# Performance work log

Hardware: AMD Instinct MI355X
Metric: run time of the kernel (lower is better)

The kernel has to match this reference:

```python
import jax, jax.numpy as jnp
import numpy as np

WS = 7       # window size
SHIFT = 3    # shift size
NH = 6       # num heads

def layernorm(x, w, b, eps=1e-5):
    mu = jnp.mean(x, axis=-1, keepdims=True)
    var = jnp.var(x, axis=-1, keepdims=True)
    return (x - mu) * jax.lax.rsqrt(var + eps) * w + b

def setup_inputs() -> dict:
    key = jax.random.key(0)
    ks = jax.random.split(key, 8)
    B, H, W, C = 16, 56, 56, 192
    hid = 4 * C
    s = lambda k, shape, fan: jax.random.normal(k, shape, jnp.float32) * (fan ** -0.5)
    return {
        "x": jax.random.normal(ks[0], (B, H, W, C), jnp.float32),
        "ln1_w": jnp.ones((C,), jnp.float32), "ln1_b": jnp.zeros((C,), jnp.float32),
        "qkv_w": s(ks[1], (C, 3 * C), C), "qkv_b": jnp.zeros((3 * C,), jnp.float32),
        "proj_w": s(ks[2], (C, C), C), "proj_b": jnp.zeros((C,), jnp.float32),
        "ln2_w": jnp.ones((C,), jnp.float32), "ln2_b": jnp.zeros((C,), jnp.float32),
        "mlp_w1": s(ks[3], (C, hid), C), "mlp_b1": jnp.zeros((hid,), jnp.float32),
        "mlp_w2": s(ks[4], (hid, C), hid), "mlp_b2": jnp.zeros((C,), jnp.float32),
    }

def reference(x, ln1_w, ln1_b, qkv_w, qkv_b, proj_w, proj_b, ln2_w, ln2_b, mlp_w1, mlp_b1, mlp_w2, mlp_b2):
    B, H, W, C = x.shape
    hd = C // NH
    scale = hd ** -0.5
    N = WS * WS

    shortcut = x
    xn = layernorm(x, ln1_w, ln1_b)
    # cyclic shift
    xs = jnp.roll(xn, shift=(-SHIFT, -SHIFT), axis=(1, 2))
    # window partition: [B*nW, N, C]
    xw = xs.reshape(B, H // WS, WS, W // WS, WS, C)
    xw = xw.transpose(0, 1, 3, 2, 4, 5).reshape(-1, N, C)

    # window attention
    qkv = xw @ qkv_w + qkv_b                       # [Bn, N, 3C]
    qkv = qkv.reshape(-1, N, 3, NH, hd).transpose(2, 0, 3, 1, 4)  # [3, Bn, NH, N, hd]
    q, k, v = qkv[0], qkv[1], qkv[2]
    attn = jnp.einsum('bhqd,bhkd->bhqk', q, k) * scale
    attn = jax.nn.softmax(attn, axis=-1)
    o = jnp.einsum('bhqk,bhkd->bhqd', attn, v)     # [Bn, NH, N, hd]
    o = o.transpose(0, 2, 1, 3).reshape(-1, N, C)
    o = o @ proj_w + proj_b

    # window reverse
    o = o.reshape(B, H // WS, W // WS, WS, WS, C)
    o = o.transpose(0, 1, 3, 2, 4, 5).reshape(B, H, W, C)
    # reverse shift
    o = jnp.roll(o, shift=(SHIFT, SHIFT), axis=(1, 2))

    x = shortcut + o
    # MLP (exact GELU, matching torch nn.GELU default)
    h = layernorm(x, ln2_w, ln2_b)
    h = jax.nn.gelu(h @ mlp_w1 + mlp_b1, approximate=False)
    x = x + (h @ mlp_w2 + mlp_b2)
    return x
```

## Files before the change

kernel.cpp:

```cpp
#include <hip/hip_runtime.h>
#include <hip/hip_bf16.h>
#include <math.h>

typedef __attribute__((ext_vector_type(8))) short short8;
typedef __attribute__((ext_vector_type(4))) float float4v;
typedef __attribute__((ext_vector_type(2))) unsigned int uint2v;

#define C_DIM 192
#define NHEADS 6
#define NTOK 50176

__device__ __forceinline__ float bf2f(unsigned short u){
  union { unsigned int i; float f; } x; x.i = ((unsigned int)u) << 16; return x.f;
}
__device__ __forceinline__ unsigned short f2bf(float f){
  union { float f; unsigned int i; } x; x.f = f;
  unsigned int r = x.i + 0x7fff + ((x.i >> 16) & 1);
  return (unsigned short)(r >> 16);
}
__device__ __forceinline__ unsigned int rbf(float f){
  union { float f; unsigned int i; } x; x.f = f;
  return x.i + 0x7fff + ((x.i >> 16) & 1);
}
__device__ __forceinline__ unsigned int pack_bf2(float lo, float hi){
  return __builtin_amdgcn_perm(rbf(hi), rbf(lo), 0x07060302);
}

__device__ __forceinline__ void gload_lds16(const unsigned short* g, unsigned short* l){
  __builtin_amdgcn_global_load_lds((const __attribute__((address_space(1))) void*)g,
                                   (__attribute__((address_space(3))) void*)l, 16, 0, 0);
}

__device__ __forceinline__ int nat_token(int r){
  int win = r / 49, n = r - win * 49;
  int b = win >> 6, rem = win & 63;
  int hs = (rem >> 3) * 7 + n / 7;
  int ws = (rem & 7) * 7 + n % 7;
  int h = hs + 3; if (h >= 56) h -= 56;
  int w = ws + 3; if (w >= 56) w -= 56;
  return (b * 56 + h) * 56 + w;
}

__device__ __forceinline__ float gelu_f(float v){
  float t = v * v;
  float u = fmaf(0.1029436f, t, 2.302208f);
  float e = __builtin_amdgcn_exp2f(-v * u);
  return v * __builtin_amdgcn_rcpf(1.f + e);
}

__global__ void transpose_kernel(const float* __restrict__ in,
                                 unsigned short* __restrict__ out, int R, int Cc){
  int idx = blockIdx.x * 256 + threadIdx.x;
  if (idx < R * Cc){ int r = idx / Cc, c = idx - r * Cc; out[(long)c * R + r] = f2bf(in[idx]); }
}

__global__ __launch_bounds__(256) void ln1_kernel(const float* __restrict__ x,
                                                  const float* __restrict__ w,
                                                  const float* __restrict__ b,
                                                  unsigned short* __restrict__ out){
  int wave = threadIdx.x >> 6, lane = threadIdx.x & 63;
  int r = blockIdx.x * 4 + wave;
  int src = nat_token(r);
  const float* xp = x + (long)src * C_DIM;
  float v0 = xp[lane], v1 = xp[lane + 64], v2 = xp[lane + 128];
  float s = v0 + v1 + v2, s2 = v0*v0 + v1*v1 + v2*v2;
  for (int m = 32; m >= 1; m >>= 1){ s += __shfl_xor(s, m, 64); s2 += __shfl_xor(s2, m, 64); }
  float mean = s * (1.f/192.f);
  float var  = s2 * (1.f/192.f) - mean*mean;
  float rs = rsqrtf(var + 1e-5f);
  unsigned short* op = out + (long)r * C_DIM;
  op[lane]       = f2bf((v0-mean)*rs*w[lane]       + b[lane]);
  op[lane + 64]  = f2bf((v1-mean)*rs*w[lane + 64]  + b[lane + 64]);
  op[lane + 128] = f2bf((v2-mean)*rs*w[lane + 128] + b[lane + 128]);
}

__global__ __launch_bounds__(256) void attn_kernel(const unsigned short* __restrict__ qkv,
                                                   unsigned short* __restrict__ o){
  __shared__ unsigned short pbuf[4][64][72];
  int wave = threadIdx.x >> 6, lane = threadIdx.x & 63;
  int quad = lane >> 4, l16 = lane & 15;
  int wid = blockIdx.x * 4 + wave;
  int win = wid / NHEADS, head = wid - win * NHEADS;
  const unsigned short* qp = qkv + (long)win * 49 * 576 + head * 32;
  const unsigned short* kp = qp + 192;
  const unsigned short* vp = qp + 384;

  short8 qa[4], kb[4];
  #pragma unroll
  for (int mi = 0; mi < 4; mi++){
    int m = mi * 16 + l16; if (m > 48) m = 48;
    qa[mi] = *(const short8*)&qp[(long)m * 576 + quad * 8];
  }
  #pragma unroll
  for (int ni = 0; ni < 4; ni++){
    int n = ni * 16 + l16; if (n > 48) n = 48;
    kb[ni] = *(const short8*)&kp[(long)n * 576 + quad * 8];
  }
  float4v S[4][4];
  #pragma unroll
  for (int mi = 0; mi < 4; mi++)
    #pragma unroll
    for (int ni = 0; ni < 4; ni++) S[mi][ni] = (float4v)0.f;
  #pragma unroll
  for (int mi = 0; mi < 4; mi++)
    #pragma unroll
    for (int ni = 0; ni < 4; ni++)
      S[mi][ni] = __builtin_amdgcn_mfma_f32_16x16x32_bf16(qa[mi], kb[ni], S[mi][ni], 0, 0, 0);

  #pragma unroll
  for (int mi = 0; mi < 4; mi++){
    #pragma unroll
    for (int r = 0; r < 4; r++){
      float e[4];
      float sum = 0.f;
      #pragma unroll
      for (int ni = 0; ni < 4; ni++){
        int n = ni * 16 + l16;
        float s = S[mi][ni][r] * 0.17677669529663687f;
        s = fminf(s, 80.f);
        float ev = (n <= 48) ? __expf(s) : 0.f;
        e[ni] = ev; sum += ev;
      }
      sum += __shfl_xor(sum, 1, 64);
      sum += __shfl_xor(sum, 2, 64);
      sum += __shfl_xor(sum, 4, 64);
      sum += __shfl_xor(sum, 8, 64);
      float inv = 1.f / sum;
      int m = mi * 16 + quad * 4 + r;
      #pragma unroll
      for (int ni = 0; ni < 4; ni++)
        pbuf[wave][m][ni * 16 + l16] = f2bf(e[ni] * inv);
    }
  }
  __syncthreads();

  short8 vb[2][2];
  #pragma unroll
  for (int kk2 = 0; kk2 < 2; kk2++){
    #pragma unroll
    for (int ni = 0; ni < 2; ni++){
      union { unsigned short us[8]; short8 v8; } u;
      #pragma unroll
      for (int j = 0; j < 8; j++){
        int k = kk2 * 32 + quad * 8 + j; if (k > 48) k = 48;
        u.us[j] = vp[(long)k * 576 + ni * 16 + l16];
      }
      vb[kk2][ni] = u.v8;
    }
  }

  float4v O[4][2];
  #pragma unroll
  for (int mi = 0; mi < 4; mi++)
    #pragma unroll
    for (int ni = 0; ni < 2; ni++) O[mi][ni] = (float4v)0.f;
  #pragma unroll
  for (int kk2 = 0; kk2 < 2; kk2++){
    short8 pa[4];
    #pragma unroll
    for (int mi = 0; mi < 4; mi++)
      pa[mi] = *(const short8*)&pbuf[wave][mi * 16 + l16][kk2 * 32 + quad * 8];
    #pragma unroll
    for (int mi = 0; mi < 4; mi++)
      #pragma unroll
      for (int ni = 0; ni < 2; ni++)
        O[mi][ni] = __builtin_amdgcn_mfma_f32_16x16x32_bf16(pa[mi], vb[kk2][ni], O[mi][ni], 0, 0, 0);
  }

  #pragma unroll
  for (int mi = 0; mi < 4; mi++){
    int m0 = mi * 16 + quad * 4;
    #pragma unroll
    for (int r = 0; r < 4; r++){
      if (m0 + r <= 48){
        #pragma unroll
        for (int ni = 0; ni < 2; ni++)
          o[((long)win * 49 + m0 + r) * C_DIM + head * 32 + ni * 16 + l16] = f2bf(O[mi][ni][r]);
      }
    }
  }
}

template<int EPI>
__global__ __launch_bounds__(256) void gemm_kernel(const unsigned short* __restrict__ A,
                                                   const unsigned short* __restrict__ Bt,
                                                   const float* __restrict__ bias,
                                                   unsigned short* __restrict__ Cout,
                                                   float* __restrict__ Fout,
                                                   const float* __restrict__ Xres,
                                                   int N, int K){
  __shared__ unsigned short As[128 * 64];
  __shared__ unsigned short Bs[64 * 64];
  int tid = threadIdx.x;
  int wave = tid >> 6, lane = tid & 63, quad = lane >> 4, l16 = lane & 15;
  int wm = (wave >> 1) * 64, wn = (wave & 1) * 32;
  int lrow = lane >> 3, lg = lane & 7;
  int gcol = (lg ^ lrow) * 8;
  float4v acc[4][2];
  #pragma unroll
  for (int i = 0; i < 4; i++)
    #pragma unroll
    for (int jj = 0; jj < 2; jj++) acc[i][jj] = (float4v)0.f;

  long arow0 = (long)blockIdx.x * 128;
  long brow0 = (long)blockIdx.y * 64;
  int sw = (l16 & 7);

  for (int k0 = 0; k0 < K; k0 += 64){
    #pragma unroll
    for (int t = 0; t < 4; t++){
      int ci = wave + 4 * t;
      gload_lds16(&A[(arow0 + ci * 8 + lrow) * (long)K + k0 + gcol], &As[ci * 512]);
    }
    #pragma unroll
    for (int t = 0; t < 2; t++){
      int ci = wave + 4 * t;
      gload_lds16(&Bt[(brow0 + ci * 8 + lrow) * (long)K + k0 + gcol], &Bs[ci * 512]);
    }
    __syncthreads();
    #pragma unroll
    for (int kk8 = 0; kk8 < 8; kk8 += 4){
      short8 a[4], b[2];
      #pragma unroll
      for (int mi = 0; mi < 4; mi++)
        a[mi] = *(const short8*)&As[(wm + mi*16 + l16) * 64 + ((quad + kk8) ^ sw) * 8];
      #pragma unroll
      for (int ni = 0; ni < 2; ni++)
        b[ni] = *(const short8*)&Bs[(wn + ni*16 + l16) * 64 + ((quad + kk8) ^ sw) * 8];
      #pragma unroll
      for (int mi = 0; mi < 4; mi++)
        #pragma unroll
        for (int ni = 0; ni < 2; ni++)
          acc[mi][ni] = __builtin_amdgcn_mfma_f32_16x16x32_bf16(b[ni], a[mi], acc[mi][ni], 0, 0, 0);
    }
    __syncthreads();
  }

  float4v bias4[2];
  #pragma unroll
  for (int ni = 0; ni < 2; ni++)
    bias4[ni] = *(const float4v*)&bias[brow0 + wn + ni*16 + quad*4];

  #pragma unroll
  for (int mi = 0; mi < 4; mi++){
    long r = arow0 + wm + mi*16 + l16;
    long tr = (EPI == 1) ? (long)nat_token((int)r) : r;
    #pragma unroll
    for (int ni = 0; ni < 2; ni++){
      long c0 = brow0 + wn + ni*16 + quad*4;
      float4v v = acc[mi][ni] + bias4[ni];
      if (EPI == 0){
        uint2v pp;
        pp[0] = pack_bf2(v[0], v[1]);
        pp[1] = pack_bf2(v[2], v[3]);
        *(uint2v*)&Cout[r * N + c0] = pp;
      } else {
        long idx = tr * C_DIM + c0;
        float4v xr = *(const float4v*)&Xres[idx];
        *(float4v*)&Fout[idx] = xr + v;
      }
    }
  }
}

__global__ __launch_bounds__(256, 4) void gemm128_kernel(const unsigned short* __restrict__ A,
                                                         const unsigned short* __restrict__ Bt,
                                                         const float* __restrict__ bias,
                                                         unsigned short* __restrict__ Cout,
                                                         int N, int K){
  __shared__ unsigned short As[128 * 64];
  __shared__ unsigned short Bs[128 * 64];
  int tid = threadIdx.x;
  int wave = tid >> 6, lane = tid & 63, quad = lane >> 4, l16 = lane & 15;
  int wm = (wave >> 1) * 64, wn = (wave & 1) * 64;
  int lrow = lane >> 3, lg = lane & 7;
  int gcol = (lg ^ lrow) * 8;
  int sw = (l16 & 7);
  float4v acc[4][4];
  #pragma unroll
  for (int i = 0; i < 4; i++)
    #pragma unroll
    for (int jj = 0; jj < 4; jj++) acc[i][jj] = (float4v)0.f;

  long arow0 = (long)blockIdx.x * 128;
  long brow0 = (long)blockIdx.y * 128;

  for (int k0 = 0; k0 < K; k0 += 64){
    #pragma unroll
    for (int t = 0; t < 4; t++){
      int ci = wave + 4 * t;
      gload_lds16(&A[(arow0 + ci * 8 + lrow) * (long)K + k0 + gcol], &As[ci * 512]);
    }
    #pragma unroll
    for (int t = 0; t < 4; t++){
      int ci = wave + 4 * t;
      gload_lds16(&Bt[(brow0 + ci * 8 + lrow) * (long)K + k0 + gcol], &Bs[ci * 512]);
    }
    __syncthreads();
    #pragma unroll
    for (int kk8 = 0; kk8 < 8; kk8 += 4){
      short8 a[4], b[4];
      #pragma unroll
      for (int mi = 0; mi < 4; mi++)
        a[mi] = *(const short8*)&As[(wm + mi*16 + l16) * 64 + ((quad + kk8) ^ sw) * 8];
      #pragma unroll
      for (int ni = 0; ni < 4; ni++)
        b[ni] = *(const short8*)&Bs[(wn + ni*16 + l16) * 64 + ((quad + kk8) ^ sw) * 8];
      #pragma unroll
      for (int mi = 0; mi < 4; mi++)
        #pragma unroll
        for (int ni = 0; ni < 4; ni++)
          acc[mi][ni] = __builtin_amdgcn_mfma_f32_16x16x32_bf16(b[ni], a[mi], acc[mi][ni], 0, 0, 0);
    }
    __syncthreads();
  }

  float4v bias4[4];
  #pragma unroll
  for (int ni = 0; ni < 4; ni++)
    bias4[ni] = *(const float4v*)&bias[brow0 + wn + ni*16 + quad*4];

  #pragma unroll
  for (int mi = 0; mi < 4; mi++){
    long r = arow0 + wm + mi*16 + l16;
    #pragma unroll
    for (int ni = 0; ni < 4; ni++){
      long c0 = brow0 + wn + ni*16 + quad*4;
      float4v v = acc[mi][ni] + bias4[ni];
      #pragma unroll
      for (int e = 0; e < 4; e++) v[e] = gelu_f(v[e]);
      uint2v pp;
      pp[0] = pack_bf2(v[0], v[1]);
      pp[1] = pack_bf2(v[2], v[3]);
      *(uint2v*)&Cout[r * N + c0] = pp;
    }
  }
}

__global__ __launch_bounds__(512, 4) void proj_ln2_kernel(const unsigned short* __restrict__ A,
                                                          const unsigned short* __restrict__ Bt,
                                                          const float* __restrict__ bias,
                                                          const float* __restrict__ x,
                                                          float* __restrict__ y,
                                                          const float* __restrict__ lnw,
                                                          const float* __restrict__ lnb,
                                                          unsigned short* __restrict__ hn){
  __shared__ unsigned short As[64 * 64];
  __shared__ unsigned short Bs[192 * 64];
  __shared__ float lnred[2][2][16][4][2];
  int tid = threadIdx.x;
  int wave = tid >> 6, lane = tid & 63, quad = lane >> 4, l16 = lane & 15;
  int wr = wave >> 2, wc = wave & 3;
  int lrow = lane >> 3, lg = lane & 7;
  int gcol = (lg ^ lrow) * 8;
  int sw = (l16 & 7);
  long arow0 = (long)blockIdx.x * 64;

  float4v acc[2][3];
  #pragma unroll
  for (int i = 0; i < 2; i++)
    #pragma unroll
    for (int j = 0; j < 3; j++) acc[i][j] = (float4v)0.f;

  for (int k0 = 0; k0 < 192; k0 += 64){
    #pragma unroll
    for (int t = 0; t < 4; t++){
      int i = wave + 8 * t;
      if (i < 8){
        gload_lds16(&A[(arow0 + i * 8 + lrow) * 192 + k0 + gcol], &As[i * 512]);
      } else {
        int ci = i - 8;
        gload_lds16(&Bt[(ci * 8 + lrow) * 192 + k0 + gcol], &Bs[ci * 512]);
      }
    }
    __syncthreads();
    #pragma unroll
    for (int kk8 = 0; kk8 < 8; kk8 += 4){
      short8 a[2], b[3];
      #pragma unroll
      for (int mi = 0; mi < 2; mi++)
        a[mi] = *(const short8*)&As[(wr*32 + mi*16 + l16) * 64 + ((quad + kk8) ^ sw) * 8];
      #pragma unroll
      for (int ni = 0; ni < 3; ni++)
        b[ni] = *(const short8*)&Bs[(wc*48 + ni*16 + l16) * 64 + ((quad + kk8) ^ sw) * 8];
      #pragma unroll
      for (int mi = 0; mi < 2; mi++)
        #pragma unroll
        for (int ni = 0; ni < 3; ni++)
          acc[mi][ni] = __builtin_amdgcn_mfma_f32_16x16x32_bf16(b[ni], a[mi], acc[mi][ni], 0, 0, 0);
    }
    if (k0 < 128) __syncthreads();
  }

  float4v bias4[3];
  #pragma unroll
  for (int ni = 0; ni < 3; ni++)
    bias4[ni] = *(const float4v*)&bias[wc*48 + ni*16 + quad*4];

  #pragma unroll
  for (int mi = 0; mi < 2; mi++){
    long rwin = arow0 + wr*32 + mi*16 + l16;
    long t = nat_token((int)rwin);
    float s = 0.f, s2 = 0.f;
    #pragma unroll
    for (int ni = 0; ni < 3; ni++){
      long idx = t * C_DIM + wc*48 + ni*16 + quad*4;
      float4v xr = *(const float4v*)&x[idx];
      float4v v = acc[mi][ni] + bias4[ni] + xr;
      *(float4v*)&y[idx] = v;
      acc[mi][ni] = v;
      #pragma unroll
      for (int e = 0; e < 4; e++){ s += v[e]; s2 += v[e]*v[e]; }
    }
    s  += __shfl_xor(s, 16, 64);  s  += __shfl_xor(s, 32, 64);
    s2 += __shfl_xor(s2, 16, 64); s2 += __shfl_xor(s2, 32, 64);
    if (quad == 0){ lnred[wr][mi][l16][wc][0] = s; lnred[wr][mi][l16][wc][1] = s2; }
  }
  __syncthreads();

  #pragma unroll
  for (int mi = 0; mi < 2; mi++){
    long rwin = arow0 + wr*32 + mi*16 + l16;
    float S = 0.f, S2 = 0.f;
    #pragma unroll
    for (int w = 0; w < 4; w++){ S += lnred[wr][mi][l16][w][0]; S2 += lnred[wr][mi][l16][w][1]; }
    float mean = S * (1.f/192.f);
    float var  = S2 * (1.f/192.f) - mean*mean;
    float rs = rsqrtf(var + 1e-5f);
    #pragma unroll
    for (int ni = 0; ni < 3; ni++){
      int c0 = wc*48 + ni*16 + quad*4;
      float4v w4 = *(const float4v*)&lnw[c0];
      float4v b4 = *(const float4v*)&lnb[c0];
      float4v v = acc[mi][ni];
      float g0 = (v[0]-mean)*rs*w4[0] + b4[0];
      float g1 = (v[1]-mean)*rs*w4[1] + b4[1];
      float g2 = (v[2]-mean)*rs*w4[2] + b4[2];
      float g3 = (v[3]-mean)*rs*w4[3] + b4[3];
      uint2v pp;
      pp[0] = pack_bf2(g0, g1);
      pp[1] = pack_bf2(g2, g3);
      *(uint2v*)&hn[rwin * C_DIM + c0] = pp;
    }
  }
}

extern "C" void kernel_launch(void* const* d_in, const int* in_sizes, int n_in,
                              void* d_out, int out_size, void* d_ws, size_t ws_size,
                              hipStream_t stream){
  const float* x      = (const float*)d_in[0];
  const float* ln1_w  = (const float*)d_in[1];
  const float* ln1_b  = (const float*)d_in[2];
  const float* qkv_w  = (const float*)d_in[3];
  const float* qkv_b  = (const float*)d_in[4];
  const float* proj_w = (const float*)d_in[5];
  const float* proj_b = (const float*)d_in[6];
  const float* ln2_w  = (const float*)d_in[7];
  const float* ln2_b  = (const float*)d_in[8];
  const float* mlp_w1 = (const float*)d_in[9];
  const float* mlp_b1 = (const float*)d_in[10];
  const float* mlp_w2 = (const float*)d_in[11];
  const float* mlp_b2 = (const float*)d_in[12];
  float* out = (float*)d_out;

  char* ws = (char*)d_ws;
  unsigned short* qkv_wt = (unsigned short*)(ws);
  unsigned short* proj_wt= (unsigned short*)(ws + 221184);
  unsigned short* w1t    = (unsigned short*)(ws + 294912);
  unsigned short* w2t    = (unsigned short*)(ws + 589824);
  unsigned short* R1     = (unsigned short*)(ws + 884736);
  unsigned short* R0     = (unsigned short*)(ws + 20152320);

  unsigned short* xw   = R1;
  unsigned short* obuf = R1;
  unsigned short* hn   = R1;
  unsigned short* qkv  = R0;
  unsigned short* hbuf = R0;

  transpose_kernel<<<(110592 + 255) / 256, 256, 0, stream>>>(qkv_w, qkv_wt, 192, 576);
  transpose_kernel<<<(36864  + 255) / 256, 256, 0, stream>>>(proj_w, proj_wt, 192, 192);
  transpose_kernel<<<(147456 + 255) / 256, 256, 0, stream>>>(mlp_w1, w1t, 192, 768);
  transpose_kernel<<<(147456 + 255) / 256, 256, 0, stream>>>(mlp_w2, w2t, 768, 192);

  ln1_kernel<<<NTOK / 4, 256, 0, stream>>>(x, ln1_w, ln1_b, xw);
  gemm_kernel<0><<<dim3(392, 9), 256, 0, stream>>>(xw, qkv_wt, qkv_b, qkv, nullptr, nullptr, 576, 192);
  attn_kernel<<<(NTOK / 49) * NHEADS / 4, 256, 0, stream>>>(qkv, obuf);
  proj_ln2_kernel<<<NTOK / 64, 512, 0, stream>>>(obuf, proj_wt, proj_b, x, out, ln2_w, ln2_b, hn);
  gemm128_kernel<<<dim3(392, 6), 256, 0, stream>>>(hn, w1t, mlp_b1, hbuf, 768, 192);
  gemm_kernel<1><<<dim3(392, 3), 256, 0, stream>>>(hbuf, w2t, mlp_b2, nullptr, out, out, 192, 768);
}
```

Baseline: 279.2 us.

## Fuse MLP fc1+GELU and fc2 into one kernel keeping hidden tile in LDS

```diff
diff --git a/kernel.cpp b/kernel.cpp
--- a/kernel.cpp
+++ b/kernel.cpp
@@ -181,13 +181,10 @@
   }
 }
 
-template<int EPI>
 __global__ __launch_bounds__(256) void gemm_kernel(const unsigned short* __restrict__ A,
                                                    const unsigned short* __restrict__ Bt,
                                                    const float* __restrict__ bias,
                                                    unsigned short* __restrict__ Cout,
-                                                   float* __restrict__ Fout,
-                                                   const float* __restrict__ Xres,
                                                    int N, int K){
   __shared__ unsigned short As[128 * 64];
   __shared__ unsigned short Bs[64 * 64];
@@ -244,91 +241,10 @@
   #pragma unroll
   for (int mi = 0; mi < 4; mi++){
     long r = arow0 + wm + mi*16 + l16;
-    long tr = (EPI == 1) ? (long)nat_token((int)r) : r;
     #pragma unroll
     for (int ni = 0; ni < 2; ni++){
       long c0 = brow0 + wn + ni*16 + quad*4;
       float4v v = acc[mi][ni] + bias4[ni];
-      if (EPI == 0){
-        uint2v pp;
-        pp[0] = pack_bf2(v[0], v[1]);
-        pp[1] = pack_bf2(v[2], v[3]);
-        *(uint2v*)&Cout[r * N + c0] = pp;
-      } else {
-        long idx = tr * C_DIM + c0;
-        float4v xr = *(const float4v*)&Xres[idx];
-        *(float4v*)&Fout[idx] = xr + v;
-      }
-    }
-  }
-}
-
-__global__ __launch_bounds__(256, 4) void gemm128_kernel(const unsigned short* __restrict__ A,
-                                                         const unsigned short* __restrict__ Bt,
-                                                         const float* __restrict__ bias,
-                                                         unsigned short* __restrict__ Cout,
-                                                         int N, int K){
-  __shared__ unsigned short As[128 * 64];
-  __shared__ unsigned short Bs[128 * 64];
-  int tid = threadIdx.x;
-  int wave = tid >> 6, lane = tid & 63, quad = lane >> 4, l16 = lane & 15;
-  int wm = (wave >> 1) * 64, wn = (wave & 1) * 64;
-  int lrow = lane >> 3, lg = lane & 7;
-  int gcol = (lg ^ lrow) * 8;
-  int sw = (l16 & 7);
-  float4v acc[4][4];
-  #pragma unroll
-  for (int i = 0; i < 4; i++)
-    #pragma unroll
-    for (int jj = 0; jj < 4; jj++) acc[i][jj] = (float4v)0.f;
-
-  long arow0 = (long)blockIdx.x * 128;
-  long brow0 = (long)blockIdx.y * 128;
-
-  for (int k0 = 0; k0 < K; k0 += 64){
-    #pragma unroll
-    for (int t = 0; t < 4; t++){
-      int ci = wave + 4 * t;
-      gload_lds16(&A[(arow0 + ci * 8 + lrow) * (long)K + k0 + gcol], &As[ci * 512]);
-    }
-    #pragma unroll
-    for (int t = 0; t < 4; t++){
-      int ci = wave + 4 * t;
-      gload_lds16(&Bt[(brow0 + ci * 8 + lrow) * (long)K + k0 + gcol], &Bs[ci * 512]);
-    }
-    __syncthreads();
-    #pragma unroll
-    for (int kk8 = 0; kk8 < 8; kk8 += 4){
-      short8 a[4], b[4];
-      #pragma unroll
-      for (int mi = 0; mi < 4; mi++)
-        a[mi] = *(const short8*)&As[(wm + mi*16 + l16) * 64 + ((quad + kk8) ^ sw) * 8];
-      #pragma unroll
-      for (int ni = 0; ni < 4; ni++)
-        b[ni] = *(const short8*)&Bs[(wn + ni*16 + l16) * 64 + ((quad + kk8) ^ sw) * 8];
-      #pragma unroll
-      for (int mi = 0; mi < 4; mi++)
-        #pragma unroll
-        for (int ni = 0; ni < 4; ni++)
-          acc[mi][ni] = __builtin_amdgcn_mfma_f32_16x16x32_bf16(b[ni], a[mi], acc[mi][ni], 0, 0, 0);
-    }
-    __syncthreads();
-  }
-
-  float4v bias4[4];
-  #pragma unroll
-  for (int ni = 0; ni < 4; ni++)
-    bias4[ni] = *(const float4v*)&bias[brow0 + wn + ni*16 + quad*4];
-
-  #pragma unroll
-  for (int mi = 0; mi < 4; mi++){
-    long r = arow0 + wm + mi*16 + l16;
-    #pragma unroll
-    for (int ni = 0; ni < 4; ni++){
-      long c0 = brow0 + wn + ni*16 + quad*4;
-      float4v v = acc[mi][ni] + bias4[ni];
-      #pragma unroll
-      for (int e = 0; e < 4; e++) v[e] = gelu_f(v[e]);
       uint2v pp;
       pp[0] = pack_bf2(v[0], v[1]);
       pp[1] = pack_bf2(v[2], v[3]);
@@ -445,6 +361,111 @@
   }
 }
 
+__global__ __launch_bounds__(256, 4) void fused_mlp_kernel(const unsigned short* __restrict__ hn,
+                                                           const unsigned short* __restrict__ w1t,
+                                                           const float* __restrict__ b1,
+                                                           const unsigned short* __restrict__ w2t,
+                                                           const float* __restrict__ b2,
+                                                           float* __restrict__ y){
+  __shared__ __attribute__((aligned(16))) unsigned short As[3 * 64 * 64];
+  __shared__ __attribute__((aligned(16))) unsigned short Hs[64 * 72];
+  int tid = threadIdx.x;
+  int wave = tid >> 6, lane = tid & 63, quad = lane >> 4, l16 = lane & 15;
+  int wm = (wave >> 1) * 32;
+  int wn1 = (wave & 1) * 32;
+  int wn2 = (wave & 1) * 96;
+  int lrow = lane >> 3, lg = lane & 7;
+  int gcol = (lg ^ lrow) * 8;
+  int sw = l16 & 7;
+  long arow0 = (long)blockIdx.x * 64;
+
+  float4v acc2[2][6];
+  #pragma unroll
+  for (int i = 0; i < 2; i++)
+    #pragma unroll
+    for (int j = 0; j < 6; j++) acc2[i][j] = (float4v)0.f;
+
+  #pragma unroll
+  for (int t = 0; t < 6; t++){
+    int i = wave + 4 * t; int gg = i >> 3, br8 = (i & 7) << 3;
+    gload_lds16(&hn[(arow0 + br8 + lrow) * C_DIM + gg * 64 + gcol], &As[gg * 4096 + br8 * 64]);
+  }
+  __syncthreads();
+
+  #pragma unroll 1
+  for (int j = 0; j < 12; j++){
+    int c0 = j * 64;
+    float4v acc1[2][2];
+    #pragma unroll
+    for (int mi = 0; mi < 2; mi++)
+      #pragma unroll
+      for (int ni = 0; ni < 2; ni++) acc1[mi][ni] = (float4v)0.f;
+    #pragma unroll
+    for (int kk = 0; kk < 6; kk++){
+      int gg = kk >> 1, xb = (kk & 1) * 4;
+      short8 a[2];
+      #pragma unroll
+      for (int mi = 0; mi < 2; mi++)
+        a[mi] = *(const short8*)&As[gg * 4096 + (wm + mi*16 + l16) * 64 + ((xb + quad) ^ sw) * 8];
+      #pragma unroll
+      for (int ni = 0; ni < 2; ni++){
+        short8 b = *(const short8*)&w1t[(long)(c0 + wn1 + ni*16 + l16) * 192 + kk*32 + quad*8];
+        #pragma unroll
+        for (int mi = 0; mi < 2; mi++)
+          acc1[mi][ni] = __builtin_amdgcn_mfma_f32_16x16x32_bf16(b, a[mi], acc1[mi][ni], 0, 0, 0);
+      }
+    }
+    #pragma unroll
+    for (int ni = 0; ni < 2; ni++){
+      float4v b14 = *(const float4v*)&b1[c0 + wn1 + ni*16 + quad*4];
+      #pragma unroll
+      for (int mi = 0; mi < 2; mi++){
+        float4v v = acc1[mi][ni] + b14;
+        #pragma unroll
+        for (int e = 0; e < 4; e++) v[e] = gelu_f(v[e]);
+        uint2v pp;
+        pp[0] = pack_bf2(v[0], v[1]);
+        pp[1] = pack_bf2(v[2], v[3]);
+        *(uint2v*)&Hs[(wm + mi*16 + l16) * 72 + wn1 + ni*16 + quad*4] = pp;
+      }
+    }
+    __syncthreads();
+
+    #pragma unroll
+    for (int kk2 = 0; kk2 < 2; kk2++){
+      short8 pa[2];
+      #pragma unroll
+      for (int mi = 0; mi < 2; mi++)
+        pa[mi] = *(const short8*)&Hs[(wm + mi*16 + l16) * 72 + kk2*32 + quad*8];
+      #pragma unroll
+      for (int ni = 0; ni < 6; ni++){
+        short8 b = *(const short8*)&w2t[(long)(wn2 + ni*16 + l16) * 768 + c0 + kk2*32 + quad*8];
+        #pragma unroll
+        for (int mi = 0; mi < 2; mi++)
+          acc2[mi][ni] = __builtin_amdgcn_mfma_f32_16x16x32_bf16(b, pa[mi], acc2[mi][ni], 0, 0, 0);
+      }
+    }
+    __syncthreads();
+  }
+
+  float4v b24[6];
+  #pragma unroll
+  for (int ni = 0; ni < 6; ni++)
+    b24[ni] = *(const float4v*)&b2[wn2 + ni*16 + quad*4];
+
+  #pragma unroll
+  for (int mi = 0; mi < 2; mi++){
+    int row = (int)(arow0 + wm + mi*16 + l16);
+    long t = nat_token(row);
+    #pragma unroll
+    for (int ni = 0; ni < 6; ni++){
+      long idx = t * C_DIM + wn2 + ni*16 + quad*4;
+      float4v xr = *(const float4v*)&y[idx];
+      *(float4v*)&y[idx] = xr + acc2[mi][ni] + b24[ni];
+    }
+  }
+}
+
 extern "C" void kernel_launch(void* const* d_in, const int* in_sizes, int n_in,
                               void* d_out, int out_size, void* d_ws, size_t ws_size,
                               hipStream_t stream){
@@ -475,7 +496,6 @@
   unsigned short* obuf = R1;
   unsigned short* hn   = R1;
   unsigned short* qkv  = R0;
-  unsigned short* hbuf = R0;
 
   transpose_kernel<<<(110592 + 255) / 256, 256, 0, stream>>>(qkv_w, qkv_wt, 192, 576);
   transpose_kernel<<<(36864  + 255) / 256, 256, 0, stream>>>(proj_w, proj_wt, 192, 192);
@@ -483,9 +503,8 @@
   transpose_kernel<<<(147456 + 255) / 256, 256, 0, stream>>>(mlp_w2, w2t, 768, 192);
 
   ln1_kernel<<<NTOK / 4, 256, 0, stream>>>(x, ln1_w, ln1_b, xw);
-  gemm_kernel<0><<<dim3(392, 9), 256, 0, stream>>>(xw, qkv_wt, qkv_b, qkv, nullptr, nullptr, 576, 192);
+  gemm_kernel<<<dim3(392, 9), 256, 0, stream>>>(xw, qkv_wt, qkv_b, qkv, 576, 192);
   attn_kernel<<<(NTOK / 49) * NHEADS / 4, 256, 0, stream>>>(qkv, obuf);
   proj_ln2_kernel<<<NTOK / 64, 512, 0, stream>>>(obuf, proj_wt, proj_b, x, out, ln2_w, ln2_b, hn);
-  gemm128_kernel<<<dim3(392, 6), 256, 0, stream>>>(hn, w1t, mlp_b1, hbuf, 768, 192);
-  gemm_kernel<1><<<dim3(392, 3), 256, 0, stream>>>(hbuf, w2t, mlp_b2, nullptr, out, out, 192, 768);
-}
+  fused_mlp_kernel<<<NTOK / 64, 256, 0, stream>>>(hn, w1t, mlp_b1, w2t, mlp_b2, out);
+}
```

Measured after the change: 336.2 us. +20.4%, slower.

## Fuse QKV projection into window attention kernel, keeping QKV in shared memory

Applied to the files above, without the earlier changes.

```diff
diff --git a/kernel.cpp b/kernel.cpp
--- a/kernel.cpp
+++ b/kernel.cpp
@@ -74,48 +74,101 @@
   op[lane + 128] = f2bf((v2-mean)*rs*w[lane + 128] + b[lane + 128]);
 }
 
-__global__ __launch_bounds__(256) void attn_kernel(const unsigned short* __restrict__ qkv,
-                                                   unsigned short* __restrict__ o){
-  __shared__ unsigned short pbuf[4][64][72];
-  int wave = threadIdx.x >> 6, lane = threadIdx.x & 63;
-  int quad = lane >> 4, l16 = lane & 15;
-  int wid = blockIdx.x * 4 + wave;
-  int win = wid / NHEADS, head = wid - win * NHEADS;
-  const unsigned short* qp = qkv + (long)win * 49 * 576 + head * 32;
-  const unsigned short* kp = qp + 192;
-  const unsigned short* vp = qp + 384;
-
-  short8 qa[4], kb[4];
-  #pragma unroll
-  for (int mi = 0; mi < 4; mi++){
-    int m = mi * 16 + l16; if (m > 48) m = 48;
-    qa[mi] = *(const short8*)&qp[(long)m * 576 + quad * 8];
+__global__ __launch_bounds__(768) void win_attn_kernel(const unsigned short* __restrict__ xw,
+                                                       const unsigned short* __restrict__ qkv_wt,
+                                                       const float* __restrict__ qkv_b,
+                                                       unsigned short* __restrict__ o){
+  __shared__ __attribute__((aligned(16))) unsigned short QKVs[64 * 584];
+  __shared__ __attribute__((aligned(16))) unsigned short Ps[12][32][72];
+  unsigned short* As = &Ps[0][0][0];
+  int tid = threadIdx.x;
+  int wave = tid >> 6, lane = tid & 63, quad = lane >> 4, l16 = lane & 15;
+  int lrow = lane >> 3, lg = lane & 7;
+  int gcol = (lg ^ lrow) * 8;
+  int sw = l16 & 7;
+  int win = blockIdx.x;
+  long arow0 = (long)win * 49;
+
+  #pragma unroll
+  for (int t = 0; t < 2; t++){
+    int i = wave + 12 * t;
+    int gg = i >> 3, br8 = (i & 7) << 3;
+    gload_lds16(&xw[(arow0 + br8 + lrow) * C_DIM + gg * 64 + gcol], &As[gg * 4096 + br8 * 64]);
+  }
+  __syncthreads();
+
+  int wcol0 = wave * 48;
+  float4v acc[4][3];
+  #pragma unroll
+  for (int i = 0; i < 4; i++)
+    #pragma unroll
+    for (int j = 0; j < 3; j++) acc[i][j] = (float4v)0.f;
+
+  #pragma unroll
+  for (int kk = 0; kk < 6; kk++){
+    int gg = kk >> 1, xb = (kk & 1) * 4;
+    short8 a[4];
+    #pragma unroll
+    for (int mi = 0; mi < 4; mi++)
+      a[mi] = *(const short8*)&As[gg * 4096 + (mi*16 + l16) * 64 + ((xb + quad) ^ sw) * 8];
+    #pragma unroll
+    for (int ni = 0; ni < 3; ni++){
+      short8 b = *(const short8*)&qkv_wt[(long)(wcol0 + ni*16 + l16) * 192 + kk*32 + quad*8];
+      #pragma unroll
+      for (int mi = 0; mi < 4; mi++)
+        acc[mi][ni] = __builtin_amdgcn_mfma_f32_16x16x32_bf16(b, a[mi], acc[mi][ni], 0, 0, 0);
+    }
+  }
+  #pragma unroll
+  for (int ni = 0; ni < 3; ni++){
+    float4v b4 = *(const float4v*)&qkv_b[wcol0 + ni*16 + quad*4];
+    #pragma unroll
+    for (int mi = 0; mi < 4; mi++){
+      float4v v = acc[mi][ni] + b4;
+      uint2v pp;
+      pp[0] = pack_bf2(v[0], v[1]);
+      pp[1] = pack_bf2(v[2], v[3]);
+      *(uint2v*)&QKVs[(mi*16 + l16) * 584 + wcol0 + ni*16 + quad*4] = pp;
+    }
+  }
+  __syncthreads();
+
+  int head = wave >> 1, half = wave & 1;
+  const unsigned short* qp = QKVs + head * 32;
+  const unsigned short* kp = QKVs + 192 + head * 32;
+  const unsigned short* vp = QKVs + 384 + head * 32;
+
+  short8 qa[2], kb[4];
+  #pragma unroll
+  for (int mi = 0; mi < 2; mi++){
+    int m = half*32 + mi*16 + l16; if (m > 48) m = 48;
+    qa[mi] = *(const short8*)&qp[m * 584 + quad * 8];
   }
   #pragma unroll
   for (int ni = 0; ni < 4; ni++){
-    int n = ni * 16 + l16; if (n > 48) n = 48;
-    kb[ni] = *(const short8*)&kp[(long)n * 576 + quad * 8];
-  }
-  float4v S[4][4];
-  #pragma unroll
-  for (int mi = 0; mi < 4; mi++)
+    int n = ni*16 + l16; if (n > 48) n = 48;
+    kb[ni] = *(const short8*)&kp[n * 584 + quad * 8];
+  }
+  float4v S[2][4];
+  #pragma unroll
+  for (int mi = 0; mi < 2; mi++)
     #pragma unroll
     for (int ni = 0; ni < 4; ni++) S[mi][ni] = (float4v)0.f;
   #pragma unroll
-  for (int mi = 0; mi < 4; mi++)
+  for (int mi = 0; mi < 2; mi++)
     #pragma unroll
     for (int ni = 0; ni < 4; ni++)
       S[mi][ni] = __builtin_amdgcn_mfma_f32_16x16x32_bf16(qa[mi], kb[ni], S[mi][ni], 0, 0, 0);
 
   #pragma unroll
-  for (int mi = 0; mi < 4; mi++){
+  for (int mi = 0; mi < 2; mi++){
     #pragma unroll
     for (int r = 0; r < 4; r++){
       float e[4];
       float sum = 0.f;
       #pragma unroll
       for (int ni = 0; ni < 4; ni++){
-        int n = ni * 16 + l16;
+        int n = ni*16 + l16;
         float s = S[mi][ni][r] * 0.17677669529663687f;
         s = fminf(s, 80.f);
         float ev = (n <= 48) ? __expf(s) : 0.f;
@@ -126,13 +179,12 @@
       sum += __shfl_xor(sum, 4, 64);
       sum += __shfl_xor(sum, 8, 64);
       float inv = 1.f / sum;
-      int m = mi * 16 + quad * 4 + r;
+      int m = mi*16 + quad*4 + r;
       #pragma unroll
       for (int ni = 0; ni < 4; ni++)
-        pbuf[wave][m][ni * 16 + l16] = f2bf(e[ni] * inv);
-    }
-  }
-  __syncthreads();
+        Ps[wave][m][ni*16 + l16] = f2bf(e[ni] * inv);
+    }
+  }
 
   short8 vb[2][2];
   #pragma unroll
@@ -142,197 +194,41 @@
       union { unsigned short us[8]; short8 v8; } u;
       #pragma unroll
       for (int j = 0; j < 8; j++){
-        int k = kk2 * 32 + quad * 8 + j; if (k > 48) k = 48;
-        u.us[j] = vp[(long)k * 576 + ni * 16 + l16];
+        int k = kk2*32 + quad*8 + j; if (k > 48) k = 48;
+        u.us[j] = vp[k * 584 + ni*16 + l16];
       }
       vb[kk2][ni] = u.v8;
     }
   }
 
-  float4v O[4][2];
-  #pragma unroll
-  for (int mi = 0; mi < 4; mi++)
+  float4v O[2][2];
+  #pragma unroll
+  for (int mi = 0; mi < 2; mi++)
     #pragma unroll
     for (int ni = 0; ni < 2; ni++) O[mi][ni] = (float4v)0.f;
   #pragma unroll
   for (int kk2 = 0; kk2 < 2; kk2++){
-    short8 pa[4];
-    #pragma unroll
-    for (int mi = 0; mi < 4; mi++)
-      pa[mi] = *(const short8*)&pbuf[wave][mi * 16 + l16][kk2 * 32 + quad * 8];
-    #pragma unroll
-    for (int mi = 0; mi < 4; mi++)
+    short8 pa[2];
+    #pragma unroll
+    for (int mi = 0; mi < 2; mi++)
+      pa[mi] = *(const short8*)&Ps[wave][mi*16 + l16][kk2*32 + quad*8];
+    #pragma unroll
+    for (int mi = 0; mi < 2; mi++)
       #pragma unroll
       for (int ni = 0; ni < 2; ni++)
         O[mi][ni] = __builtin_amdgcn_mfma_f32_16x16x32_bf16(pa[mi], vb[kk2][ni], O[mi][ni], 0, 0, 0);
   }
 
   #pragma unroll
-  for (int mi = 0; mi < 4; mi++){
-    int m0 = mi * 16 + quad * 4;
+  for (int mi = 0; mi < 2; mi++){
+    int m0 = half*32 + mi*16 + quad*4;
     #pragma unroll
     for (int r = 0; r < 4; r++){
       if (m0 + r <= 48){
         #pragma unroll
         for (int ni = 0; ni < 2; ni++)
-          o[((long)win * 49 + m0 + r) * C_DIM + head * 32 + ni * 16 + l16] = f2bf(O[mi][ni][r]);
+          o[(arow0 + m0 + r) * C_DIM + head*32 + ni*16 + l16] = f2bf(O[mi][ni][r]);
       }
-    }
-  }
-}
-
-template<int EPI>
-__global__ __launch_bounds__(256) void gemm_kernel(const unsigned short* __restrict__ A,
-                                                   const unsigned short* __restrict__ Bt,
-                                                   const float* __restrict__ bias,
-                                                   unsigned short* __restrict__ Cout,
-                                                   float* __restrict__ Fout,
-                                                   const float* __restrict__ Xres,
-                                                   int N, int K){
-  __shared__ unsigned short As[128 * 64];
-  __shared__ unsigned short Bs[64 * 64];
-  int tid = threadIdx.x;
-  int wave = tid >> 6, lane = tid & 63, quad = lane >> 4, l16 = lane & 15;
-  int wm = (wave >> 1) * 64, wn = (wave & 1) * 32;
-  int lrow = lane >> 3, lg = lane & 7;
-  int gcol = (lg ^ lrow) * 8;
-  float4v acc[4][2];
-  #pragma unroll
-  for (int i = 0; i < 4; i++)
-    #pragma unroll
-    for (int jj = 0; jj < 2; jj++) acc[i][jj] = (float4v)0.f;
-
-  long arow0 = (long)blockIdx.x * 128;
-  long brow0 = (long)blockIdx.y * 64;
-  int sw = (l16 & 7);
-
-  for (int k0 = 0; k0 < K; k0 += 64){
-    #pragma unroll
-    for (int t = 0; t < 4; t++){
-      int ci = wave + 4 * t;
-      gload_lds16(&A[(arow0 + ci * 8 + lrow) * (long)K + k0 + gcol], &As[ci * 512]);
-    }
-    #pragma unroll
-    for (int t = 0; t < 2; t++){
-      int ci = wave + 4 * t;
-      gload_lds16(&Bt[(brow0 + ci * 8 + lrow) * (long)K + k0 + gcol], &Bs[ci * 512]);
-    }
-    __syncthreads();
-    #pragma unroll
-    for (int kk8 = 0; kk8 < 8; kk8 += 4){
-      short8 a[4], b[2];
-      #pragma unroll
-      for (int mi = 0; mi < 4; mi++)
-        a[mi] = *(const short8*)&As[(wm + mi*16 + l16) * 64 + ((quad + kk8) ^ sw) * 8];
-      #pragma unroll
-      for (int ni = 0; ni < 2; ni++)
-        b[ni] = *(const short8*)&Bs[(wn + ni*16 + l16) * 64 + ((quad + kk8) ^ sw) * 8];
-      #pragma unroll
-      for (int mi = 0; mi < 4; mi++)
-        #pragma unroll
-        for (int ni = 0; ni < 2; ni++)
-          acc[mi][ni] = __builtin_amdgcn_mfma_f32_16x16x32_bf16(b[ni], a[mi], acc[mi][ni], 0, 0, 0);
-    }
-    __syncthreads();
-  }
-
-  float4v bias4[2];
-  #pragma unroll
-  for (int ni = 0; ni < 2; ni++)
-    bias4[ni] = *(const float4v*)&bias[brow0 + wn + ni*16 + quad*4];
-
-  #pragma unroll
-  for (int mi = 0; mi < 4; mi++){
-    long r = arow0 + wm + mi*16 + l16;
-    long tr = (EPI == 1) ? (long)nat_token((int)r) : r;
-    #pragma unroll
-    for (int ni = 0; ni < 2; ni++){
-      long c0 = brow0 + wn + ni*16 + quad*4;
-      float4v v = acc[mi][ni] + bias4[ni];
-      if (EPI == 0){
-        uint2v pp;
-        pp[0] = pack_bf2(v[0], v[1]);
-        pp[1] = pack_bf2(v[2], v[3]);
-        *(uint2v*)&Cout[r * N + c0] = pp;
-      } else {
-        long idx = tr * C_DIM + c0;
-        float4v xr = *(const float4v*)&Xres[idx];
-        *(float4v*)&Fout[idx] = xr + v;
-      }
-    }
-  }
-}
-
-__global__ __launch_bounds__(256, 4) void gemm128_kernel(const unsigned short* __restrict__ A,
-                                                         const unsigned short* __restrict__ Bt,
-                                                         const float* __restrict__ bias,
-                                                         unsigned short* __restrict__ Cout,
-                                                         int N, int K){
-  __shared__ unsigned short As[128 * 64];
-  __shared__ unsigned short Bs[128 * 64];
-  int tid = threadIdx.x;
-  int wave = tid >> 6, lane = tid & 63, quad = lane >> 4, l16 = lane & 15;
-  int wm = (wave >> 1) * 64, wn = (wave & 1) * 64;
-  int lrow = lane >> 3, lg = lane & 7;
-  int gcol = (lg ^ lrow) * 8;
-  int sw = (l16 & 7);
-  float4v acc[4][4];
-  #pragma unroll
-  for (int i = 0; i < 4; i++)
-    #pragma unroll
-    for (int jj = 0; jj < 4; jj++) acc[i][jj] = (float4v)0.f;
-
-  long arow0 = (long)blockIdx.x * 128;
-  long brow0 = (long)blockIdx.y * 128;
-
-  for (int k0 = 0; k0 < K; k0 += 64){
-    #pragma unroll
-    for (int t = 0; t < 4; t++){
-      int ci = wave + 4 * t;
-      gload_lds16(&A[(arow0 + ci * 8 + lrow) * (long)K + k0 + gcol], &As[ci * 512]);
-    }
-    #pragma unroll
-    for (int t = 0; t < 4; t++){
-      int ci = wave + 4 * t;
-      gload_lds16(&Bt[(brow0 + ci * 8 + lrow) * (long)K + k0 + gcol], &Bs[ci * 512]);
-    }
-    __syncthreads();
-    #pragma unroll
-    for (int kk8 = 0; kk8 < 8; kk8 += 4){
-      short8 a[4], b[4];
-      #pragma unroll
-      for (int mi = 0; mi < 4; mi++)
-        a[mi] = *(const short8*)&As[(wm + mi*16 + l16) * 64 + ((quad + kk8) ^ sw) * 8];
-      #pragma unroll
-      for (int ni = 0; ni < 4; ni++)
-        b[ni] = *(const short8*)&Bs[(wn + ni*16 + l16) * 64 + ((quad + kk8) ^ sw) * 8];
-      #pragma unroll
-      for (int mi = 0; mi < 4; mi++)
-        #pragma unroll
-        for (int ni = 0; ni < 4; ni++)
-          acc[mi][ni] = __builtin_amdgcn_mfma_f32_16x16x32_bf16(b[ni], a[mi], acc[mi][ni], 0, 0, 0);
-    }
-    __syncthreads();
-  }
-
-  float4v bias4[4];
-  #pragma unroll
-  for (int ni = 0; ni < 4; ni++)
-    bias4[ni] = *(const float4v*)&bias[brow0 + wn + ni*16 + quad*4];
-
-  #pragma unroll
-  for (int mi = 0; mi < 4; mi++){
-    long r = arow0 + wm + mi*16 + l16;
-    #pragma unroll
-    for (int ni = 0; ni < 4; ni++){
-      long c0 = brow0 + wn + ni*16 + quad*4;
-      float4v v = acc[mi][ni] + bias4[ni];
-      #pragma unroll
-      for (int e = 0; e < 4; e++) v[e] = gelu_f(v[e]);
-      uint2v pp;
-      pp[0] = pack_bf2(v[0], v[1]);
-      pp[1] = pack_bf2(v[2], v[3]);
-      *(uint2v*)&Cout[r * N + c0] = pp;
     }
   }
 }
@@ -445,6 +341,152 @@
   }
 }
 
+__global__ __launch_bounds__(256, 4) void gemm128_kernel(const unsigned short* __restrict__ A,
+                                                         const unsigned short* __restrict__ Bt,
+                                                         const float* __restrict__ bias,
+                                                         unsigned short* __restrict__ Cout,
+                                                         int N, int K){
+  __shared__ unsigned short As[128 * 64];
+  __shared__ unsigned short Bs[128 * 64];
+  int tid = threadIdx.x;
+  int wave = tid >> 6, lane = tid & 63, quad = lane >> 4, l16 = lane & 15;
+  int wm = (wave >> 1) * 64, wn = (wave & 1) * 64;
+  int lrow = lane >> 3, lg = lane & 7;
+  int gcol = (lg ^ lrow) * 8;
+  int sw = (l16 & 7);
+  float4v acc[4][4];
+  #pragma unroll
+  for (int i = 0; i < 4; i++)
+    #pragma unroll
+    for (int jj = 0; jj < 4; jj++) acc[i][jj] = (float4v)0.f;
+
+  long arow0 = (long)blockIdx.x * 128;
+  long brow0 = (long)blockIdx.y * 128;
+
+  for (int k0 = 0; k0 < K; k0 += 64){
+    #pragma unroll
+    for (int t = 0; t < 4; t++){
+      int ci = wave + 4 * t;
+      gload_lds16(&A[(arow0 + ci * 8 + lrow) * (long)K + k0 + gcol], &As[ci * 512]);
+    }
+    #pragma unroll
+    for (int t = 0; t < 4; t++){
+      int ci = wave + 4 * t;
+      gload_lds16(&Bt[(brow0 + ci * 8 + lrow) * (long)K + k0 + gcol], &Bs[ci * 512]);
+    }
+    __syncthreads();
+    #pragma unroll
+    for (int kk8 = 0; kk8 < 8; kk8 += 4){
+      short8 a[4], b[4];
+      #pragma unroll
+      for (int mi = 0; mi < 4; mi++)
+        a[mi] = *(const short8*)&As[(wm + mi*16 + l16) * 64 + ((quad + kk8) ^ sw) * 8];
+      #pragma unroll
+      for (int ni = 0; ni < 4; ni++)
+        b[ni] = *(const short8*)&Bs[(wn + ni*16 + l16) * 64 + ((quad + kk8) ^ sw) * 8];
+      #pragma unroll
+      for (int mi = 0; mi < 4; mi++)
+        #pragma unroll
+        for (int ni = 0; ni < 4; ni++)
+          acc[mi][ni] = __builtin_amdgcn_mfma_f32_16x16x32_bf16(b[ni], a[mi], acc[mi][ni], 0, 0, 0);
+    }
+    __syncthreads();
+  }
+
+  float4v bias4[4];
+  #pragma unroll
+  for (int ni = 0; ni < 4; ni++)
+    bias4[ni] = *(const float4v*)&bias[brow0 + wn + ni*16 + quad*4];
+
+  #pragma unroll
+  for (int mi = 0; mi < 4; mi++){
+    long r = arow0 + wm + mi*16 + l16;
+    #pragma unroll
+    for (int ni = 0; ni < 4; ni++){
+      long c0 = brow0 + wn + ni*16 + quad*4;
+      float4v v = acc[mi][ni] + bias4[ni];
+      #pragma unroll
+      for (int e = 0; e < 4; e++) v[e] = gelu_f(v[e]);
+      uint2v pp;
+      pp[0] = pack_bf2(v[0], v[1]);
+      pp[1] = pack_bf2(v[2], v[3]);
+      *(uint2v*)&Cout[r * N + c0] = pp;
+    }
+  }
+}
+
+__global__ __launch_bounds__(256) void gemm_rmw_kernel(const unsigned short* __restrict__ A,
+                                                       const unsigned short* __restrict__ Bt,
+                                                       const float* __restrict__ bias,
+                                                       float* __restrict__ Fout,
+                                                       const float* __restrict__ Xres,
+                                                       int K){
+  __shared__ unsigned short As[128 * 64];
+  __shared__ unsigned short Bs[64 * 64];
+  int tid = threadIdx.x;
+  int wave = tid >> 6, lane = tid & 63, quad = lane >> 4, l16 = lane & 15;
+  int wm = (wave >> 1) * 64, wn = (wave & 1) * 32;
+  int lrow = lane >> 3, lg = lane & 7;
+  int gcol = (lg ^ lrow) * 8;
+  float4v acc[4][2];
+  #pragma unroll
+  for (int i = 0; i < 4; i++)
+    #pragma unroll
+    for (int jj = 0; jj < 2; jj++) acc[i][jj] = (float4v)0.f;
+
+  long arow0 = (long)blockIdx.x * 128;
+  long brow0 = (long)blockIdx.y * 64;
+  int sw = (l16 & 7);
+
+  for (int k0 = 0; k0 < K; k0 += 64){
+    #pragma unroll
+    for (int t = 0; t < 4; t++){
+      int ci = wave + 4 * t;
+      gload_lds16(&A[(arow0 + ci * 8 + lrow) * (long)K + k0 + gcol], &As[ci * 512]);
+    }
+    #pragma unroll
+    for (int t = 0; t < 2; t++){
+      int ci = wave + 4 * t;
+      gload_lds16(&Bt[(brow0 + ci * 8 + lrow) * (long)K + k0 + gcol], &Bs[ci * 512]);
+    }
+    __syncthreads();
+    #pragma unroll
+    for (int kk8 = 0; kk8 < 8; kk8 += 4){
+      short8 a[4], b[2];
+      #pragma unroll
+      for (int mi = 0; mi < 4; mi++)
+        a[mi] = *(const short8*)&As[(wm + mi*16 + l16) * 64 + ((quad + kk8) ^ sw) * 8];
+      #pragma unroll
+      for (int ni = 0; ni < 2; ni++)
+        b[ni] = *(const short8*)&Bs[(wn + ni*16 + l16) * 64 + ((quad + kk8) ^ sw) * 8];
+      #pragma unroll
+      for (int mi = 0; mi < 4; mi++)
+        #pragma unroll
+        for (int ni = 0; ni < 2; ni++)
+          acc[mi][ni] = __builtin_amdgcn_mfma_f32_16x16x32_bf16(b[ni], a[mi], acc[mi][ni], 0, 0, 0);
+    }
+    __syncthreads();
+  }
+
+  float4v bias4[2];
+  #pragma unroll
+  for (int ni = 0; ni < 2; ni++)
+    bias4[ni] = *(const float4v*)&bias[brow0 + wn + ni*16 + quad*4];
+
+  #pragma unroll
+  for (int mi = 0; mi < 4; mi++){
+    long r = arow0 + wm + mi*16 + l16;
+    long tr = (long)nat_token((int)r);
+    #pragma unroll
+    for (int ni = 0; ni < 2; ni++){
+      long c0 = brow0 + wn + ni*16 + quad*4;
+      long idx = tr * C_DIM + c0;
+      float4v xr = *(const float4v*)&Xres[idx];
+      *(float4v*)&Fout[idx] = xr + acc[mi][ni] + bias4[ni];
+    }
+  }
+}
+
 extern "C" void kernel_launch(void* const* d_in, const int* in_sizes, int n_in,
                               void* d_out, int out_size, void* d_ws, size_t ws_size,
                               hipStream_t stream){
@@ -472,9 +514,8 @@
   unsigned short* R0     = (unsigned short*)(ws + 20152320);
 
   unsigned short* xw   = R1;
-  unsigned short* obuf = R1;
   unsigned short* hn   = R1;
-  unsigned short* qkv  = R0;
+  unsigned short* obuf = R0;
   unsigned short* hbuf = R0;
 
   transpose_kernel<<<(110592 + 255) / 256, 256, 0, stream>>>(qkv_w, qkv_wt, 192, 576);
@@ -483,9 +524,8 @@
   transpose_kernel<<<(147456 + 255) / 256, 256, 0, stream>>>(mlp_w2, w2t, 768, 192);
 
   ln1_kernel<<<NTOK / 4, 256, 0, stream>>>(x, ln1_w, ln1_b, xw);
-  gemm_kernel<0><<<dim3(392, 9), 256, 0, stream>>>(xw, qkv_wt, qkv_b, qkv, nullptr, nullptr, 576, 192);
-  attn_kernel<<<(NTOK / 49) * NHEADS / 4, 256, 0, stream>>>(qkv, obuf);
+  win_attn_kernel<<<NTOK / 49, 768, 0, stream>>>(xw, qkv_wt, qkv_b, obuf);
   proj_ln2_kernel<<<NTOK / 64, 512, 0, stream>>>(obuf, proj_wt, proj_b, x, out, ln2_w, ln2_b, hn);
   gemm128_kernel<<<dim3(392, 6), 256, 0, stream>>>(hn, w1t, mlp_b1, hbuf, 768, 192);
-  gemm_kernel<1><<<dim3(392, 3), 256, 0, stream>>>(hbuf, w2t, mlp_b2, nullptr, out, out, 192, 768);
-}
+  gemm_rmw_kernel<<<dim3(392, 3), 256, 0, stream>>>(hbuf, w2t, mlp_b2, out, out, 768);
+}
```

Result: no change. 276.0 us (-1.1%).
